# Optimization experiments

Measured on AMD Instinct MI355X. Metric: run time of the kernel, lower is better.

The kernel has to match this reference:

```python
import jax, jax.numpy as jnp
import numpy as np

M_GROUP = 8  # VENOM m: pattern period along in_features

def _nm_mask(in_features, dtype):
    # NMVectorSparsifier.get_random_mask keeps positions 0 and 2 of every group of m=8
    pat = jnp.array([1.0, 0.0, 1.0, 0.0, 0.0, 0.0, 0.0, 0.0], dtype=dtype)
    return jnp.tile(pat, in_features // M_GROUP)  # [in_features]


def setup_inputs() -> dict:
    key = jax.random.key(0)
    k1, k2, k3 = jax.random.split(key, 3)
    B, S, D_IN, D_OUT = 8, 2048, 4096, 4096
    x = jax.random.normal(k1, (B, S, D_IN), dtype=jnp.float32)
    weight = jax.random.normal(k2, (D_OUT, D_IN), dtype=jnp.float32) * 0.02
    bias = jax.random.normal(k3, (D_OUT,), dtype=jnp.float32) * 0.02
    return {"x": x, "weight": weight, "bias": bias}


def reference(x, weight, bias):
    # y = x @ (W * mask)^T + b  -- N:M (2:8) vector-sparse linear, dense-math reference
    mask = _nm_mask(weight.shape[1], weight.dtype)  # [D_IN]
    w = weight * mask[None, :]                      # [D_OUT, D_IN]
    return jnp.einsum('bsd,od->bso', x, w) + bias
```

## Files before the change

### kernel.cpp

```cpp
#include <hip/hip_runtime.h>
#include <hip/hip_bf16.h>
#include <stdint.h>

#define MROWS 16384
#define DIN   4096
#define DOUT  4096
#define KEFF  1024

typedef __attribute__((ext_vector_type(8))) __bf16 bf16x8;
typedef __attribute__((ext_vector_type(4))) float f32x4;

#define AS1 __attribute__((address_space(1)))
#define AS3 __attribute__((address_space(3)))

__device__ __forceinline__ uint32_t f2bf_rne(float f) {
  union { float f; uint32_t u; } v; v.f = f;
  uint32_t u = v.u;
  return (u + 0x7fffu + ((u >> 16) & 1u)) >> 16;
}

__global__ void venom_gather2(const float* __restrict__ src,
                              uint2* __restrict__ dst, int npairs) {
  int stride = gridDim.x * blockDim.x;
  for (int i = blockIdx.x * blockDim.x + threadIdx.x; i < npairs; i += stride) {
    const float4* p = reinterpret_cast<const float4*>(src) + (size_t)i * 4;
    float4 a = p[0];
    float4 b = p[2];
    uint2 r;
    r.x = f2bf_rne(a.x) | (f2bf_rne(a.z) << 16);
    r.y = f2bf_rne(b.x) | (f2bf_rne(b.z) << 16);
    dst[i] = r;
  }
}

#define BM 256
#define BN 256
#define BK 64
#define NT (KEFF / BK)
#define TPB 4

__device__ __forceinline__ int swz_off(int R, int lg) {
  int sr = R >> 1;
  return sr * 128 + (((((R & 1) << 2) | lg) ^ (sr & 7)) << 4);
}

__global__ __launch_bounds__(512, 2) void venom_gemm(
    const __bf16* __restrict__ A, const __bf16* __restrict__ Bm,
    const float* __restrict__ bias, float* __restrict__ C) {
  __shared__ __bf16 As[2][2][128 * 64];
  __shared__ __bf16 Bs[2][2][128 * 64];

  int nwg = gridDim.x;
  int cpx = nwg >> 3;
  int bid = blockIdx.x;
  int swz = (bid & 7) * cpx + (bid >> 3);
  int mblk = swz >> 2;
  int ngrp = swz & 3;

  int t = threadIdx.x;
  int wid = t >> 6, l = t & 63;
  int wr = wid >> 2, wc = wid & 3;
  int lr = l & 15, lg = l >> 4;

  const __bf16* Ag = A + (size_t)(mblk * BM) * KEFF;

  float biasr[TPB][4];
  #pragma unroll
  for (int j = 0; j < TPB; ++j)
    #pragma unroll
    for (int ni = 0; ni < 4; ++ni)
      biasr[j][ni] = bias[(ngrp * TPB + j) * BN + wc * 64 + ni * 16 + lr];

  f32x4 acc[8][4] = {};

  auto stage_half = [&](int j2, int kt2, int kh) {
    const int buf = kt2 & 1;
    const __bf16* Bg = Bm + (size_t)((ngrp * TPB + j2) * BN) * KEFF;
    const int k0 = kt2 * BK + kh * 32;
    #pragma unroll
    for (int i = 0; i < 2; ++i) {
      int e = i * 512 + t;
      int sr = e >> 3;
      int s = (e & 7) ^ (sr & 7);
      int row = sr * 2 + (s >> 2);
      int koff = (s & 3) * 8;
      __builtin_amdgcn_global_load_lds(
          (const AS1 uint32_t*)(Ag + (size_t)row * KEFF + k0 + koff),
          ((AS3 uint32_t*)&As[buf][kh][0]) + e * 4, 16, 0, 0);
      __builtin_amdgcn_global_load_lds(
          (const AS1 uint32_t*)(Bg + (size_t)row * KEFF + k0 + koff),
          ((AS3 uint32_t*)&Bs[buf][kh][0]) + e * 4, 16, 0, 0);
    }
  };

  stage_half(0, 0, 0);
  stage_half(0, 0, 1);
  asm volatile("s_waitcnt vmcnt(4)" ::: "memory");
  __builtin_amdgcn_s_barrier();

  bf16x8 bfrag[4];

  #pragma unroll
  for (int j = 0; j < TPB; ++j) {
    #pragma unroll 1
    for (int kt = 0; kt < NT; ++kt) {
      const int cur = kt & 1;
      const bool last_it = (j == TPB - 1) && (kt == NT - 1);
      const int j2  = (kt < NT - 1) ? j : j + 1;
      const int kt2 = (kt < NT - 1) ? kt + 1 : 0;

      #pragma unroll
      for (int ph = 0; ph < 4; ++ph) {
        const int mh = ph & 1, kh = ph >> 1;
        const char* aB = (const char*)&As[cur][kh][0];
        bf16x8 af[4];
        #pragma unroll
        for (int mi = 0; mi < 4; ++mi)
          af[mi] = *(const bf16x8*)(aB + swz_off(wr * 128 + mh * 64 + mi * 16 + lr, lg));
        if (mh == 0) {
          const char* bB = (const char*)&Bs[cur][kh][0];
          #pragma unroll
          for (int ni = 0; ni < 4; ++ni)
            bfrag[ni] = *(const bf16x8*)(bB + swz_off(wc * 64 + ni * 16 + lr, lg));
          if (!last_it) stage_half(j2, kt2, kh);
        }

        __builtin_amdgcn_s_barrier();
        __builtin_amdgcn_s_setprio(1);
        #pragma unroll
        for (int mi = 0; mi < 4; ++mi)
          #pragma unroll
          for (int ni = 0; ni < 4; ++ni)
            acc[mh * 4 + mi][ni] = __builtin_amdgcn_mfma_f32_16x16x32_bf16(
                af[mi], bfrag[ni], acc[mh * 4 + mi][ni], 0, 0, 0);
        __builtin_amdgcn_s_setprio(0);

        if (ph == 1) {
          if (!last_it) asm volatile("s_waitcnt vmcnt(4)" ::: "memory");
          else          asm volatile("s_waitcnt vmcnt(0)" ::: "memory");
          __builtin_amdgcn_s_barrier();
        } else if (ph == 3) {
          if (!last_it) {
            asm volatile("s_waitcnt vmcnt(4)" ::: "memory");
            __builtin_amdgcn_s_barrier();
          }
        } else {
          __builtin_amdgcn_s_barrier();
        }
      }
    }

    {
      int colbase = (ngrp * TPB + j) * BN + wc * 64;
      int rowbase = mblk * BM + wr * 128;
      #pragma unroll
      for (int mh = 0; mh < 2; ++mh)
        #pragma unroll
        for (int mi = 0; mi < 4; ++mi) {
          int row0 = rowbase + mh * 64 + mi * 16 + lg * 4;
          #pragma unroll
          for (int ni = 0; ni < 4; ++ni) {
            int col = colbase + ni * 16 + lr;
            f32x4 cv = acc[mh * 4 + mi][ni];
            #pragma unroll
            for (int jj = 0; jj < 4; ++jj)
              C[(size_t)(row0 + jj) * DOUT + col] = cv[jj] + biasr[j][ni];
          }
        }
      #pragma unroll
      for (int q = 0; q < 8; ++q)
        #pragma unroll
        for (int ni = 0; ni < 4; ++ni)
          acc[q][ni] = (f32x4){0.f, 0.f, 0.f, 0.f};
    }
  }
}

__global__ void venom_naive(const float* __restrict__ x, const float* __restrict__ w,
                            const float* __restrict__ bias, float* __restrict__ out) {
  size_t total = (size_t)MROWS * DOUT;
  size_t stride = (size_t)gridDim.x * blockDim.x;
  for (size_t idx = (size_t)blockIdx.x * blockDim.x + threadIdx.x; idx < total;
       idx += stride) {
    int m = (int)(idx / DOUT), n = (int)(idx % DOUT);
    const float* xr = x + (size_t)m * DIN;
    const float* wr = w + (size_t)n * DIN;
    float s = 0.f;
    for (int g = 0; g < DIN / 8; ++g)
      s += xr[g * 8] * wr[g * 8] + xr[g * 8 + 2] * wr[g * 8 + 2];
    out[idx] = s + bias[n];
  }
}

extern "C" void kernel_launch(void* const* d_in, const int* in_sizes, int n_in,
                              void* d_out, int out_size, void* d_ws, size_t ws_size,
                              hipStream_t stream) {
  const float* x    = (const float*)d_in[0];
  const float* wgt  = (const float*)d_in[1];
  const float* bias = (const float*)d_in[2];
  float* out = (float*)d_out;

  const size_t xg_bytes = (size_t)MROWS * KEFF * 2;
  const size_t wg_bytes = (size_t)DOUT * KEFF * 2;

  if (ws_size < xg_bytes + wg_bytes) {
    venom_naive<<<2048, 256, 0, stream>>>(x, wgt, bias, out);
    return;
  }

  uint32_t* xg = (uint32_t*)d_ws;
  uint32_t* wg = (uint32_t*)((char*)d_ws + xg_bytes);

  venom_gather2<<<2048, 256, 0, stream>>>(x, (uint2*)xg, MROWS * (DIN / 16));
  venom_gather2<<<1024, 256, 0, stream>>>(wgt, (uint2*)wg, DOUT * (DIN / 16));

  venom_gemm<<<(MROWS / BM) * (DOUT / BN / TPB), 512, 0, stream>>>(
      (const __bf16*)xg, (const __bf16*)wg, bias, out);
}
```

Baseline: 281.8 us.

## Double-buffer LDS fragment reads with inline asm and merge gather kernels

The GEMM main loop now prefetches the next A/B register fragments with inline ds_read_b128 while the current MFMA block runs, using explicit lgkmcnt waits to overlap LDS reads with matrix math. The two gather kernels are merged into one launch to save a launch and its tail. Bias is now loaded from global memory in the epilogue instead of being held in registers for the whole kernel. Risks are higher register pressure from the duplicate fragment buffers and fragile hand-placed waitcnt values that have to match the actual number of outstanding loads.

Result: slower. 308.9 us (+9.6%).

```diff
diff --git a/kernel.cpp b/kernel.cpp
--- a/kernel.cpp
+++ b/kernel.cpp
@@ -9,6 +9,7 @@
 
 typedef __attribute__((ext_vector_type(8))) __bf16 bf16x8;
 typedef __attribute__((ext_vector_type(4))) float f32x4;
+typedef __attribute__((ext_vector_type(4))) int   i32x4;
 
 #define AS1 __attribute__((address_space(1)))
 #define AS3 __attribute__((address_space(3)))
@@ -19,17 +20,23 @@
   return (u + 0x7fffu + ((u >> 16) & 1u)) >> 16;
 }
 
-__global__ void venom_gather2(const float* __restrict__ src,
-                              uint2* __restrict__ dst, int npairs) {
+__global__ void venom_gather_all(const float* __restrict__ x,
+                                 const float* __restrict__ w,
+                                 uint2* __restrict__ xg, uint2* __restrict__ wg) {
+  const int PX = MROWS * (DIN / 16);
+  const int PW = DOUT * (DIN / 16);
   int stride = gridDim.x * blockDim.x;
-  for (int i = blockIdx.x * blockDim.x + threadIdx.x; i < npairs; i += stride) {
-    const float4* p = reinterpret_cast<const float4*>(src) + (size_t)i * 4;
+  for (int i = blockIdx.x * blockDim.x + threadIdx.x; i < PX + PW; i += stride) {
+    const float* src; uint2* dst; int idx;
+    if (i < PX) { src = x; dst = xg; idx = i; }
+    else        { src = w; dst = wg; idx = i - PX; }
+    const float4* p = reinterpret_cast<const float4*>(src) + (size_t)idx * 4;
     float4 a = p[0];
     float4 b = p[2];
     uint2 r;
     r.x = f2bf_rne(a.x) | (f2bf_rne(a.z) << 16);
     r.y = f2bf_rne(b.x) | (f2bf_rne(b.z) << 16);
-    dst[i] = r;
+    dst[idx] = r;
   }
 }
 
@@ -38,13 +45,24 @@
 #define BK 64
 #define NT (KEFF / BK)
 #define TPB 4
-
-__device__ __forceinline__ int swz_off(int R, int lg) {
+#define HALF_BYTES 16384
+
+__device__ __forceinline__ uint32_t swz_off(int R, int lg) {
   int sr = R >> 1;
-  return sr * 128 + (((((R & 1) << 2) | lg) ^ (sr & 7)) << 4);
-}
-
-__global__ __launch_bounds__(512, 2) void venom_gemm(
+  return (uint32_t)(sr * 128 + (((((R & 1) << 2) | lg) ^ (sr & 7)) << 4));
+}
+
+__device__ __forceinline__ bf16x8 asbf(i32x4 v) {
+  union { i32x4 i; bf16x8 b; } u; u.i = v; return u.b;
+}
+
+#define DSR(dst, a) asm volatile("ds_read_b128 %0, %1" : "=v"(dst) : "v"(a))
+#define WAIT_LGKM(n) do { asm volatile("s_waitcnt lgkmcnt(" #n ")" ::: "memory"); \
+                          __builtin_amdgcn_sched_barrier(0); } while (0)
+#define WAIT_VM(n) asm volatile("s_waitcnt vmcnt(" #n ")" ::: "memory")
+#define BAR() __builtin_amdgcn_s_barrier()
+
+__global__ __launch_bounds__(512, 2) void venom_gemm_dbf(
     const __bf16* __restrict__ A, const __bf16* __restrict__ Bm,
     const float* __restrict__ bias, float* __restrict__ C) {
   __shared__ __bf16 As[2][2][128 * 64];
@@ -64,14 +82,34 @@
 
   const __bf16* Ag = A + (size_t)(mblk * BM) * KEFF;
 
-  float biasr[TPB][4];
-  #pragma unroll
-  for (int j = 0; j < TPB; ++j)
+  uint32_t asB = (uint32_t)(uintptr_t)(AS3 __bf16*)&As[0][0][0];
+  uint32_t bsB = (uint32_t)(uintptr_t)(AS3 __bf16*)&Bs[0][0][0];
+
+  f32x4 acc[8][4] = {};
+  i32x4 af0[4], af1[4], bf0[4], bf1[4];
+
+  auto issueA = [&](i32x4 (&d)[4], int buf, int kh, int mh) {
+    uint32_t base = asB + (uint32_t)((buf * 2 + kh) * HALF_BYTES);
+    #pragma unroll
+    for (int mi = 0; mi < 4; ++mi)
+      DSR(d[mi], base + swz_off(wr * 128 + mh * 64 + mi * 16 + lr, lg));
+  };
+  auto issueB = [&](i32x4 (&d)[4], int buf, int kh) {
+    uint32_t base = bsB + (uint32_t)((buf * 2 + kh) * HALF_BYTES);
     #pragma unroll
     for (int ni = 0; ni < 4; ++ni)
-      biasr[j][ni] = bias[(ngrp * TPB + j) * BN + wc * 64 + ni * 16 + lr];
-
-  f32x4 acc[8][4] = {};
+      DSR(d[ni], base + swz_off(wc * 64 + ni * 16 + lr, lg));
+  };
+  auto mfma16 = [&](int rb, i32x4 (&a)[4], i32x4 (&b)[4]) {
+    __builtin_amdgcn_s_setprio(1);
+    #pragma unroll
+    for (int mi = 0; mi < 4; ++mi)
+      #pragma unroll
+      for (int ni = 0; ni < 4; ++ni)
+        acc[rb + mi][ni] = __builtin_amdgcn_mfma_f32_16x16x32_bf16(
+            asbf(a[mi]), asbf(b[ni]), acc[rb + mi][ni], 0, 0, 0);
+    __builtin_amdgcn_s_setprio(0);
+  };
 
   auto stage_half = [&](int j2, int kt2, int kh) {
     const int buf = kt2 & 1;
@@ -95,58 +133,50 @@
 
   stage_half(0, 0, 0);
   stage_half(0, 0, 1);
-  asm volatile("s_waitcnt vmcnt(4)" ::: "memory");
-  __builtin_amdgcn_s_barrier();
-
-  bf16x8 bfrag[4];
+  WAIT_VM(4);
+  BAR();
+  issueA(af0, 0, 0, 0);
+  issueB(bf0, 0, 0);
 
   #pragma unroll
   for (int j = 0; j < TPB; ++j) {
     #pragma unroll 1
     for (int kt = 0; kt < NT; ++kt) {
       const int cur = kt & 1;
-      const bool last_it = (j == TPB - 1) && (kt == NT - 1);
+      const bool last = (j == TPB - 1) && (kt == NT - 1);
       const int j2  = (kt < NT - 1) ? j : j + 1;
       const int kt2 = (kt < NT - 1) ? kt + 1 : 0;
-
-      #pragma unroll
-      for (int ph = 0; ph < 4; ++ph) {
-        const int mh = ph & 1, kh = ph >> 1;
-        const char* aB = (const char*)&As[cur][kh][0];
-        bf16x8 af[4];
-        #pragma unroll
-        for (int mi = 0; mi < 4; ++mi)
-          af[mi] = *(const bf16x8*)(aB + swz_off(wr * 128 + mh * 64 + mi * 16 + lr, lg));
-        if (mh == 0) {
-          const char* bB = (const char*)&Bs[cur][kh][0];
-          #pragma unroll
-          for (int ni = 0; ni < 4; ++ni)
-            bfrag[ni] = *(const bf16x8*)(bB + swz_off(wc * 64 + ni * 16 + lr, lg));
-          if (!last_it) stage_half(j2, kt2, kh);
-        }
-
-        __builtin_amdgcn_s_barrier();
-        __builtin_amdgcn_s_setprio(1);
-        #pragma unroll
-        for (int mi = 0; mi < 4; ++mi)
-          #pragma unroll
-          for (int ni = 0; ni < 4; ++ni)
-            acc[mh * 4 + mi][ni] = __builtin_amdgcn_mfma_f32_16x16x32_bf16(
-                af[mi], bfrag[ni], acc[mh * 4 + mi][ni], 0, 0, 0);
-        __builtin_amdgcn_s_setprio(0);
-
-        if (ph == 1) {
-          if (!last_it) asm volatile("s_waitcnt vmcnt(4)" ::: "memory");
-          else          asm volatile("s_waitcnt vmcnt(0)" ::: "memory");
-          __builtin_amdgcn_s_barrier();
-        } else if (ph == 3) {
-          if (!last_it) {
-            asm volatile("s_waitcnt vmcnt(4)" ::: "memory");
-            __builtin_amdgcn_s_barrier();
-          }
-        } else {
-          __builtin_amdgcn_s_barrier();
-        }
+      const int nbuf = kt2 & 1;
+
+      issueA(af1, cur, 0, 1);
+      if (!last) stage_half(j2, kt2, 0);
+      BAR();
+      WAIT_LGKM(4);
+      mfma16(0, af0, bf0);
+      if (last) WAIT_VM(0); else WAIT_VM(4);
+      BAR();
+
+      issueA(af0, cur, 1, 0);
+      issueB(bf1, cur, 1);
+      BAR();
+      WAIT_LGKM(8);
+      mfma16(4, af1, bf0);
+      BAR();
+
+      issueA(af1, cur, 1, 1);
+      if (!last) stage_half(j2, kt2, 1);
+      BAR();
+      WAIT_LGKM(4);
+      mfma16(0, af0, bf1);
+      BAR();
+
+      WAIT_LGKM(0);
+      mfma16(4, af1, bf1);
+      if (last) WAIT_VM(0); else WAIT_VM(4);
+      BAR();
+      if (!last) {
+        issueA(af0, nbuf, 0, 0);
+        issueB(bf0, nbuf, 0);
       }
     }
 
@@ -154,19 +184,20 @@
       int colbase = (ngrp * TPB + j) * BN + wc * 64;
       int rowbase = mblk * BM + wr * 128;
       #pragma unroll
-      for (int mh = 0; mh < 2; ++mh)
+      for (int ni = 0; ni < 4; ++ni) {
+        int col = colbase + ni * 16 + lr;
+        float bv = bias[col];
         #pragma unroll
-        for (int mi = 0; mi < 4; ++mi) {
-          int row0 = rowbase + mh * 64 + mi * 16 + lg * 4;
+        for (int mh = 0; mh < 2; ++mh)
           #pragma unroll
-          for (int ni = 0; ni < 4; ++ni) {
-            int col = colbase + ni * 16 + lr;
+          for (int mi = 0; mi < 4; ++mi) {
+            int row0 = rowbase + mh * 64 + mi * 16 + lg * 4;
             f32x4 cv = acc[mh * 4 + mi][ni];
             #pragma unroll
             for (int jj = 0; jj < 4; ++jj)
-              C[(size_t)(row0 + jj) * DOUT + col] = cv[jj] + biasr[j][ni];
+              C[(size_t)(row0 + jj) * DOUT + col] = cv[jj] + bv;
           }
-        }
+      }
       #pragma unroll
       for (int q = 0; q < 8; ++q)
         #pragma unroll
@@ -211,9 +242,8 @@
   uint32_t* xg = (uint32_t*)d_ws;
   uint32_t* wg = (uint32_t*)((char*)d_ws + xg_bytes);
 
-  venom_gather2<<<2048, 256, 0, stream>>>(x, (uint2*)xg, MROWS * (DIN / 16));
-  venom_gather2<<<1024, 256, 0, stream>>>(wgt, (uint2*)wg, DOUT * (DIN / 16));
-
-  venom_gemm<<<(MROWS / BM) * (DOUT / BN / TPB), 512, 0, stream>>>(
+  venom_gather_all<<<2048, 256, 0, stream>>>(x, wgt, (uint2*)xg, (uint2*)wg);
+
+  venom_gemm_dbf<<<(MROWS / BM) * (DOUT / BN / TPB), 512, 0, stream>>>(
       (const __bf16*)xg, (const __bf16*)wg, bias, out);
 }
```

## Deepen GEMM prefetch pipeline and merge the two gather kernels

Applied to the files above, without the earlier changes.

The GEMM now flattens the (tile, k-step) loop into a linear stage index. It issues loads one and a half stages ahead (three half-stages in flight) instead of one stage ahead, with vmcnt waits adjusted to match. The aim is to hide more global-to-LDS latency behind MFMA work. The two bf16 gather launches are also merged into a single kernel to save a launch and the tail idle time between them. The deeper prefetch reuses the same double-buffered LDS halves, so correctness depends on the barrier placement keeping overwrites safe.

Result: no change. 287.0 us (+1.9%).

```diff
diff --git a/kernel.cpp b/kernel.cpp
--- a/kernel.cpp
+++ b/kernel.cpp
@@ -19,17 +19,23 @@
   return (u + 0x7fffu + ((u >> 16) & 1u)) >> 16;
 }
 
-__global__ void venom_gather2(const float* __restrict__ src,
-                              uint2* __restrict__ dst, int npairs) {
+__global__ void venom_gather_all(const float* __restrict__ x,
+                                 const float* __restrict__ w,
+                                 uint2* __restrict__ xg, uint2* __restrict__ wg) {
+  const int PX = MROWS * (DIN / 16);
+  const int PW = DOUT * (DIN / 16);
   int stride = gridDim.x * blockDim.x;
-  for (int i = blockIdx.x * blockDim.x + threadIdx.x; i < npairs; i += stride) {
-    const float4* p = reinterpret_cast<const float4*>(src) + (size_t)i * 4;
+  for (int i = blockIdx.x * blockDim.x + threadIdx.x; i < PX + PW; i += stride) {
+    const float* src; uint2* dst; int idx;
+    if (i < PX) { src = x; dst = xg; idx = i; }
+    else        { src = w; dst = wg; idx = i - PX; }
+    const float4* p = reinterpret_cast<const float4*>(src) + (size_t)idx * 4;
     float4 a = p[0];
     float4 b = p[2];
     uint2 r;
     r.x = f2bf_rne(a.x) | (f2bf_rne(a.z) << 16);
     r.y = f2bf_rne(b.x) | (f2bf_rne(b.z) << 16);
-    dst[i] = r;
+    dst[idx] = r;
   }
 }
 
@@ -38,13 +44,17 @@
 #define BK 64
 #define NT (KEFF / BK)
 #define TPB 4
+#define LTOT (NT * TPB)
 
 __device__ __forceinline__ int swz_off(int R, int lg) {
   int sr = R >> 1;
   return sr * 128 + (((((R & 1) << 2) | lg) ^ (sr & 7)) << 4);
 }
 
-__global__ __launch_bounds__(512, 2) void venom_gemm(
+#define WAIT_VM(n) asm volatile("s_waitcnt vmcnt(" #n ")" ::: "memory")
+#define BAR() __builtin_amdgcn_s_barrier()
+
+__global__ __launch_bounds__(512, 2) void venom_gemm_p3(
     const __bf16* __restrict__ A, const __bf16* __restrict__ Bm,
     const float* __restrict__ bias, float* __restrict__ C) {
   __shared__ __bf16 As[2][2][128 * 64];
@@ -73,8 +83,10 @@
 
   f32x4 acc[8][4] = {};
 
-  auto stage_half = [&](int j2, int kt2, int kh) {
-    const int buf = kt2 & 1;
+  auto stage_half = [&](int L2, int kh) {
+    const int buf = L2 & 1;
+    const int j2 = L2 >> 4;
+    const int kt2 = L2 & (NT - 1);
     const __bf16* Bg = Bm + (size_t)((ngrp * TPB + j2) * BN) * KEFF;
     const int k0 = kt2 * BK + kh * 32;
     #pragma unroll
@@ -93,10 +105,11 @@
     }
   };
 
-  stage_half(0, 0, 0);
-  stage_half(0, 0, 1);
-  asm volatile("s_waitcnt vmcnt(4)" ::: "memory");
-  __builtin_amdgcn_s_barrier();
+  stage_half(0, 0);
+  stage_half(0, 1);
+  stage_half(1, 0);
+  WAIT_VM(8);
+  BAR();
 
   bf16x8 bfrag[4];
 
@@ -104,10 +117,8 @@
   for (int j = 0; j < TPB; ++j) {
     #pragma unroll 1
     for (int kt = 0; kt < NT; ++kt) {
+      const int L = j * NT + kt;
       const int cur = kt & 1;
-      const bool last_it = (j == TPB - 1) && (kt == NT - 1);
-      const int j2  = (kt < NT - 1) ? j : j + 1;
-      const int kt2 = (kt < NT - 1) ? kt + 1 : 0;
 
       #pragma unroll
       for (int ph = 0; ph < 4; ++ph) {
@@ -122,10 +133,11 @@
           #pragma unroll
           for (int ni = 0; ni < 4; ++ni)
             bfrag[ni] = *(const bf16x8*)(bB + swz_off(wc * 64 + ni * 16 + lr, lg));
-          if (!last_it) stage_half(j2, kt2, kh);
+          if (kh == 0) { if (L + 1 < LTOT) stage_half(L + 1, 1); }
+          else         { if (L + 2 < LTOT) stage_half(L + 2, 0); }
         }
 
-        __builtin_amdgcn_s_barrier();
+        BAR();
         __builtin_amdgcn_s_setprio(1);
         #pragma unroll
         for (int mi = 0; mi < 4; ++mi)
@@ -136,16 +148,16 @@
         __builtin_amdgcn_s_setprio(0);
 
         if (ph == 1) {
-          if (!last_it) asm volatile("s_waitcnt vmcnt(4)" ::: "memory");
-          else          asm volatile("s_waitcnt vmcnt(0)" ::: "memory");
-          __builtin_amdgcn_s_barrier();
+          if (L <= LTOT - 2) WAIT_VM(8);
+          else               WAIT_VM(0);
+          BAR();
         } else if (ph == 3) {
-          if (!last_it) {
-            asm volatile("s_waitcnt vmcnt(4)" ::: "memory");
-            __builtin_amdgcn_s_barrier();
-          }
+          if (L <= LTOT - 3)      WAIT_VM(8);
+          else if (L == LTOT - 2) WAIT_VM(4);
+          else                    WAIT_VM(0);
+          BAR();
         } else {
-          __builtin_amdgcn_s_barrier();
+          BAR();
         }
       }
     }
@@ -211,9 +223,8 @@
   uint32_t* xg = (uint32_t*)d_ws;
   uint32_t* wg = (uint32_t*)((char*)d_ws + xg_bytes);
 
-  venom_gather2<<<2048, 256, 0, stream>>>(x, (uint2*)xg, MROWS * (DIN / 16));
-  venom_gather2<<<1024, 256, 0, stream>>>(wgt, (uint2*)wg, DOUT * (DIN / 16));
-
-  venom_gemm<<<(MROWS / BM) * (DOUT / BN / TPB), 512, 0, stream>>>(
+  venom_gather_all<<<2048, 256, 0, stream>>>(x, wgt, (uint2*)xg, (uint2*)wg);
+
+  venom_gemm_p3<<<(MROWS / BM) * (DOUT / BN / TPB), 512, 0, stream>>>(
       (const __bf16*)xg, (const __bf16*)wg, bias, out);
 }
```

## Fuse gather/convert kernels into GEMM with a grid-wide atomic barrier

Applied to the files above, without the earlier changes.

Merges the two bf16 gather/convert kernels and the GEMM into one persistent launch of 256 workgroups. Each block first gathers its slice of x and W into the workspace, then all blocks wait on a global atomic counter before starting the GEMM. This removes two kernel launches and the gaps between them. The grid barrier only works if all 256 blocks are resident at once, and it adds a memset plus spin-wait cost.

After: 420.0 us. 1.49x slower.

```diff
diff --git a/kernel.cpp b/kernel.cpp
--- a/kernel.cpp
+++ b/kernel.cpp
@@ -17,20 +17,6 @@
   union { float f; uint32_t u; } v; v.f = f;
   uint32_t u = v.u;
   return (u + 0x7fffu + ((u >> 16) & 1u)) >> 16;
-}
-
-__global__ void venom_gather2(const float* __restrict__ src,
-                              uint2* __restrict__ dst, int npairs) {
-  int stride = gridDim.x * blockDim.x;
-  for (int i = blockIdx.x * blockDim.x + threadIdx.x; i < npairs; i += stride) {
-    const float4* p = reinterpret_cast<const float4*>(src) + (size_t)i * 4;
-    float4 a = p[0];
-    float4 b = p[2];
-    uint2 r;
-    r.x = f2bf_rne(a.x) | (f2bf_rne(a.z) << 16);
-    r.y = f2bf_rne(b.x) | (f2bf_rne(b.z) << 16);
-    dst[i] = r;
-  }
 }
 
 #define BM 256
@@ -44,20 +30,69 @@
   return sr * 128 + (((((R & 1) << 2) | lg) ^ (sr & 7)) << 4);
 }
 
-__global__ __launch_bounds__(512, 2) void venom_gemm(
-    const __bf16* __restrict__ A, const __bf16* __restrict__ Bm,
-    const float* __restrict__ bias, float* __restrict__ C) {
+#define WAIT_VM(n) asm volatile("s_waitcnt vmcnt(" #n ")" ::: "memory")
+#define BAR() __builtin_amdgcn_s_barrier()
+
+__global__ __launch_bounds__(512, 2) void venom_fused(
+    const float* __restrict__ x, const float* __restrict__ w,
+    const float* __restrict__ bias, float* __restrict__ C,
+    uint32_t* __restrict__ xgw, uint32_t* __restrict__ wgw,
+    uint32_t* __restrict__ ctr) {
   __shared__ __bf16 As[2][2][128 * 64];
   __shared__ __bf16 Bs[2][2][128 * 64];
 
+  const int t = threadIdx.x;
+  const int bid = blockIdx.x;
+
+  {
+    const int PX = MROWS * (DIN / 16);
+    const int PW = DOUT * (DIN / 16);
+    const int xpb = PX / 256;
+    const int wpb = PW / 256;
+    uint2* xg2 = (uint2*)xgw;
+    uint2* wg2 = (uint2*)wgw;
+    #pragma unroll 4
+    for (int i = t; i < xpb; i += 512) {
+      int idx = bid * xpb + i;
+      const float4* p = reinterpret_cast<const float4*>(x) + (size_t)idx * 4;
+      float4 a = p[0], b = p[2];
+      uint2 r;
+      r.x = f2bf_rne(a.x) | (f2bf_rne(a.z) << 16);
+      r.y = f2bf_rne(b.x) | (f2bf_rne(b.z) << 16);
+      xg2[idx] = r;
+    }
+    #pragma unroll 4
+    for (int i = t; i < wpb; i += 512) {
+      int idx = bid * wpb + i;
+      const float4* p = reinterpret_cast<const float4*>(w) + (size_t)idx * 4;
+      float4 a = p[0], b = p[2];
+      uint2 r;
+      r.x = f2bf_rne(a.x) | (f2bf_rne(a.z) << 16);
+      r.y = f2bf_rne(b.x) | (f2bf_rne(b.z) << 16);
+      wg2[idx] = r;
+    }
+  }
+
+  WAIT_VM(0);
+  __threadfence();
+  __syncthreads();
+  if (t == 0) {
+    __hip_atomic_fetch_add(ctr, 1u, __ATOMIC_ACQ_REL, __HIP_MEMORY_SCOPE_AGENT);
+    while (__hip_atomic_load(ctr, __ATOMIC_ACQUIRE, __HIP_MEMORY_SCOPE_AGENT) <
+           (uint32_t)gridDim.x)
+      __builtin_amdgcn_s_sleep(8);
+  }
+  __syncthreads();
+
+  const __bf16* A  = (const __bf16*)xgw;
+  const __bf16* Bm = (const __bf16*)wgw;
+
   int nwg = gridDim.x;
   int cpx = nwg >> 3;
-  int bid = blockIdx.x;
   int swz = (bid & 7) * cpx + (bid >> 3);
   int mblk = swz >> 2;
   int ngrp = swz & 3;
 
-  int t = threadIdx.x;
   int wid = t >> 6, l = t & 63;
   int wr = wid >> 2, wc = wid & 3;
   int lr = l & 15, lg = l >> 4;
@@ -95,8 +130,8 @@
 
   stage_half(0, 0, 0);
   stage_half(0, 0, 1);
-  asm volatile("s_waitcnt vmcnt(4)" ::: "memory");
-  __builtin_amdgcn_s_barrier();
+  WAIT_VM(4);
+  BAR();
 
   bf16x8 bfrag[4];
 
@@ -125,7 +160,7 @@
           if (!last_it) stage_half(j2, kt2, kh);
         }
 
-        __builtin_amdgcn_s_barrier();
+        BAR();
         __builtin_amdgcn_s_setprio(1);
         #pragma unroll
         for (int mi = 0; mi < 4; ++mi)
@@ -136,16 +171,16 @@
         __builtin_amdgcn_s_setprio(0);
 
         if (ph == 1) {
-          if (!last_it) asm volatile("s_waitcnt vmcnt(4)" ::: "memory");
-          else          asm volatile("s_waitcnt vmcnt(0)" ::: "memory");
-          __builtin_amdgcn_s_barrier();
+          if (!last_it) WAIT_VM(4);
+          else          WAIT_VM(0);
+          BAR();
         } else if (ph == 3) {
           if (!last_it) {
-            asm volatile("s_waitcnt vmcnt(4)" ::: "memory");
-            __builtin_amdgcn_s_barrier();
+            WAIT_VM(4);
+            BAR();
           }
         } else {
-          __builtin_amdgcn_s_barrier();
+          BAR();
         }
       }
     }
@@ -202,18 +237,18 @@
 
   const size_t xg_bytes = (size_t)MROWS * KEFF * 2;
   const size_t wg_bytes = (size_t)DOUT * KEFF * 2;
-
-  if (ws_size < xg_bytes + wg_bytes) {
+  const size_t ctr_off  = xg_bytes + wg_bytes;
+
+  if (ws_size < ctr_off + 128) {
     venom_naive<<<2048, 256, 0, stream>>>(x, wgt, bias, out);
     return;
   }
 
-  uint32_t* xg = (uint32_t*)d_ws;
-  uint32_t* wg = (uint32_t*)((char*)d_ws + xg_bytes);
-
-  venom_gather2<<<2048, 256, 0, stream>>>(x, (uint2*)xg, MROWS * (DIN / 16));
-  venom_gather2<<<1024, 256, 0, stream>>>(wgt, (uint2*)wg, DOUT * (DIN / 16));
-
-  venom_gemm<<<(MROWS / BM) * (DOUT / BN / TPB), 512, 0, stream>>>(
-      (const __bf16*)xg, (const __bf16*)wg, bias, out);
-}
+  uint32_t* xg  = (uint32_t*)d_ws;
+  uint32_t* wg  = (uint32_t*)((char*)d_ws + xg_bytes);
+  uint32_t* ctr = (uint32_t*)((char*)d_ws + ctr_off);
+
+  hipMemsetAsync(ctr, 0, sizeof(uint32_t), stream);
+
+  venom_fused<<<256, 512, 0, stream>>>(x, wgt, bias, out, xg, wg, ctr);
+}
```
